# Performance work log

Hardware: AMD Instinct MI355X
Metric: run time of the kernel (lower is better)

The kernel has to match this reference:

```python
import jax, jax.numpy as jnp
import numpy as np

IGNORE_INDEX = -100


def setup_inputs() -> dict:
    key = jax.random.key(0)
    k1, k2, k3 = jax.random.split(key, 3)
    B, S, D, V = 4, 2048, 2048, 32000
    hidden_states = jax.random.normal(k1, (B, S, D), dtype=jnp.float32)
    lm_head_weight = jax.random.normal(k2, (V, D), dtype=jnp.float32) * (D ** -0.5)
    labels = jax.random.randint(k3, (B, S), 0, V, dtype=jnp.int64)
    return {"hidden_states": hidden_states, "lm_head_weight": lm_head_weight, "labels": labels}


def reference(hidden_states, lm_head_weight, labels):
    D = hidden_states.shape[-1]
    # causal LM shift: predict token t+1 from hidden state t
    h = hidden_states[..., :-1, :].astype(jnp.float32).reshape(-1, D)   # [N, D]
    t = labels[..., 1:].reshape(-1)                                     # [N]
    w = lm_head_weight.astype(jnp.float32)                              # [V, D]

    logits = jnp.einsum("nd,vd->nv", h, w)                              # [N, V]
    lse = jax.nn.logsumexp(logits, axis=-1)                             # [N]

    valid = t != IGNORE_INDEX
    safe_t = jnp.where(valid, t, 0)
    gold = jnp.take_along_axis(logits, safe_t[:, None], axis=-1)[:, 0]  # [N]

    nll = jnp.where(valid, lse - gold, 0.0)
    n_valid = jnp.maximum(jnp.sum(valid.astype(jnp.float32)), 1.0)
    return jnp.sum(nll) / n_valid
```

## Files before the change

kernel.cpp:

```cpp
#include <hip/hip_runtime.h>
#include <hip/hip_bf16.h>
#include <stdint.h>

#define IGNORE_INDEX (-100)

typedef __attribute__((ext_vector_type(8))) short bf16x8;
typedef __attribute__((ext_vector_type(4))) float f32x4;

static constexpr int Bv = 4, Sv = 2048, Dv = 2048, Vv = 32000;
static constexpr int Nv = Bv * (Sv - 1);
static constexpr int NP = 8192;
static constexpr int TILE = 128;
static constexpr int BK = 64;

typedef const __attribute__((address_space(1))) unsigned int* gptr_t;
typedef __attribute__((address_space(3))) unsigned int* lptr_t;

__device__ __forceinline__ unsigned short f2bf(float f) {
    unsigned int u = __float_as_uint(f);
    u += 0x7fffu + ((u >> 16) & 1u);
    return (unsigned short)(u >> 16);
}

__global__ void convert_w_kernel(const float* __restrict__ w,
                                 unsigned short* __restrict__ wbf) {
    int i = blockIdx.x * blockDim.x + threadIdx.x;
    const float4 v = ((const float4*)w)[i];
    ushort4 o;
    o.x = f2bf(v.x); o.y = f2bf(v.y); o.z = f2bf(v.z); o.w = f2bf(v.w);
    ((ushort4*)wbf)[i] = o;
}

__global__ void convert_h_kernel(const float* __restrict__ h,
                                 unsigned short* __restrict__ hbf) {
    int i = blockIdx.x * blockDim.x + threadIdx.x;
    int e0 = i * 4;
    int n = e0 >> 11;
    int d = e0 & 2047;
    ushort4 o;
    if (n < Nv) {
        int b = n / 2047;
        int s = n - b * 2047;
        const float4 v = *(const float4*)(h + ((size_t)b * Sv + s) * Dv + d);
        o.x = f2bf(v.x); o.y = f2bf(v.y); o.z = f2bf(v.z); o.w = f2bf(v.w);
    } else {
        o.x = 0; o.y = 0; o.z = 0; o.w = 0;
    }
    ((ushort4*)hbf)[i] = o;
}

__global__ void prep_meta_kernel(const int* __restrict__ labels,
                                 int* __restrict__ t,
                                 float* __restrict__ sumexp,
                                 float* __restrict__ gold) {
    int n = blockIdx.x * blockDim.x + threadIdx.x;
    if (n >= NP) return;
    sumexp[n] = 0.0f;
    gold[n] = 0.0f;
    int tv = IGNORE_INDEX;
    if (n < Nv) {
        int b = n / 2047;
        int s = n - b * 2047;
        tv = labels[b * Sv + s + 1];
    }
    t[n] = tv;
}

__global__ __launch_bounds__(256, 2)
void ce_gemm(const unsigned short* __restrict__ hbf,
             const unsigned short* __restrict__ wbf,
             const int* __restrict__ t,
             float* __restrict__ sumexp,
             float* __restrict__ gold) {
    __shared__ unsigned short lds_a[TILE * BK];
    __shared__ unsigned short lds_b[TILE * BK];
    __shared__ float lds_rowsum[TILE];
    __shared__ int lds_t[TILE];

    const int tid  = threadIdx.x;
    const int lane = tid & 63;
    const int wave = tid >> 6;
    const int r    = wave >> 1;
    const int c    = wave & 1;
    const int quad = lane >> 4;
    const int l15  = lane & 15;
    const int R0   = blockIdx.x * TILE;
    const int C0   = blockIdx.y * TILE;

    f32x4 acc[4][4];
    const f32x4 z = {0.f, 0.f, 0.f, 0.f};
#pragma unroll
    for (int mi = 0; mi < 4; ++mi)
#pragma unroll
        for (int ni = 0; ni < 4; ++ni)
            acc[mi][ni] = z;

    const int ld_r = tid >> 3;
    const int jg   = (tid & 7) ^ (ld_r & 7);
    const int ld_c = jg * 8;
    const unsigned short* ga = hbf + (size_t)(R0 + ld_r) * Dv + ld_c;
    const unsigned short* gb = wbf + (size_t)(C0 + ld_r) * Dv + ld_c;
    unsigned short* la = lds_a + tid * 8;
    unsigned short* lb = lds_b + tid * 8;

    for (int k0 = 0; k0 < Dv; k0 += BK) {
        __syncthreads();
#pragma unroll
        for (int i = 0; i < 4; ++i) {
            __builtin_amdgcn_global_load_lds(
                (gptr_t)(ga + (size_t)i * 32 * Dv + k0),
                (lptr_t)(la + i * 2048), 16, 0, 0);
            __builtin_amdgcn_global_load_lds(
                (gptr_t)(gb + (size_t)i * 32 * Dv + k0),
                (lptr_t)(lb + i * 2048), 16, 0, 0);
        }
        __syncthreads();
#pragma unroll
        for (int ks = 0; ks < BK; ks += 32) {
            bf16x8 af[4], bfr[4];
            const int cbase = quad + (ks >> 3);
#pragma unroll
            for (int mi = 0; mi < 4; ++mi) {
                const int arow = r * 64 + mi * 16 + l15;
                af[mi] = *(const bf16x8*)(lds_a + arow * BK + ((cbase ^ (arow & 7)) * 8));
            }
#pragma unroll
            for (int ni = 0; ni < 4; ++ni) {
                const int brow = c * 64 + ni * 16 + l15;
                bfr[ni] = *(const bf16x8*)(lds_b + brow * BK + ((cbase ^ (brow & 7)) * 8));
            }
#pragma unroll
            for (int mi = 0; mi < 4; ++mi)
#pragma unroll
                for (int ni = 0; ni < 4; ++ni)
                    acc[mi][ni] = __builtin_amdgcn_mfma_f32_16x16x32_bf16(
                        af[mi], bfr[ni], acc[mi][ni], 0, 0, 0);
        }
    }

    __syncthreads();
    if (tid < TILE) {
        lds_rowsum[tid] = 0.0f;
        lds_t[tid] = t[R0 + tid];
    }
    __syncthreads();

#pragma unroll
    for (int mi = 0; mi < 4; ++mi) {
#pragma unroll
        for (int reg = 0; reg < 4; ++reg) {
            const int lrow = r * 64 + mi * 16 + quad * 4 + reg;
            const int grow = R0 + lrow;
            const int lbl  = lds_t[lrow];
            float s = 0.0f;
#pragma unroll
            for (int ni = 0; ni < 4; ++ni) {
                const float v = acc[mi][ni][reg];
                s += __expf(v);
                const int gcol = C0 + c * 64 + ni * 16 + l15;
                if (lbl == gcol) gold[grow] = v;
            }
#pragma unroll
            for (int off = 1; off < 16; off <<= 1)
                s += __shfl_xor(s, off, 64);
            if (l15 == 0) atomicAdd(&lds_rowsum[lrow], s);
        }
    }
    __syncthreads();
    if (tid < TILE) {
        const int grow = R0 + tid;
        if (grow < Nv) atomicAdd(&sumexp[grow], lds_rowsum[tid]);
    }
}

__global__ void ce_finalize(const float* __restrict__ sumexp,
                            const float* __restrict__ gold,
                            const int* __restrict__ t,
                            float* __restrict__ out) {
    __shared__ float ssum[4];
    __shared__ float scnt[4];
    float s = 0.0f, cnt = 0.0f;
    for (int n = threadIdx.x; n < Nv; n += 256) {
        if (t[n] != IGNORE_INDEX) {
            s += logf(sumexp[n]) - gold[n];
            cnt += 1.0f;
        }
    }
#pragma unroll
    for (int off = 32; off > 0; off >>= 1) {
        s += __shfl_down(s, off, 64);
        cnt += __shfl_down(cnt, off, 64);
    }
    const int wid = threadIdx.x >> 6;
    if ((threadIdx.x & 63) == 0) { ssum[wid] = s; scnt[wid] = cnt; }
    __syncthreads();
    if (threadIdx.x == 0) {
        float S = 0.0f, C = 0.0f;
        for (int i = 0; i < 4; ++i) { S += ssum[i]; C += scnt[i]; }
        out[0] = S / fmaxf(C, 1.0f);
    }
}

extern "C" void kernel_launch(void* const* d_in, const int* in_sizes, int n_in,
                              void* d_out, int out_size, void* d_ws, size_t ws_size,
                              hipStream_t stream) {
    const float* h      = (const float*)d_in[0];
    const float* w      = (const float*)d_in[1];
    const int*   labels = (const int*)d_in[2];
    float* out = (float*)d_out;

    char* ws = (char*)d_ws;
    unsigned short* hbf = (unsigned short*)ws;
    unsigned short* wbf = (unsigned short*)(ws + (size_t)NP * Dv * 2);
    char* tail = ws + (size_t)NP * Dv * 2 + (size_t)Vv * Dv * 2;
    float* sumexp = (float*)tail;
    float* gold   = (float*)(tail + (size_t)NP * 4);
    int*   t      = (int*)(tail + (size_t)NP * 8);

    hipLaunchKernelGGL(convert_w_kernel, dim3((Vv * Dv / 4) / 256), dim3(256), 0, stream, w, wbf);
    hipLaunchKernelGGL(convert_h_kernel, dim3((NP * Dv / 4) / 256), dim3(256), 0, stream, h, hbf);
    hipLaunchKernelGGL(prep_meta_kernel, dim3(NP / 256), dim3(256), 0, stream, labels, t, sumexp, gold);
    hipLaunchKernelGGL(ce_gemm, dim3(NP / TILE, Vv / TILE), dim3(256), 0, stream,
                       hbf, wbf, t, sumexp, gold);
    hipLaunchKernelGGL(ce_finalize, dim3(1), dim3(256), 0, stream, sumexp, gold, t, out);
}
```

Measured before the change: 1.361 ms.

## Switch CE GEMM from bf16 to scaled FP8 MFMA 32x32x64

Converts hidden states and weights to FP8 (e4m3, with weights pre-scaled by 32) instead of bf16, and replaces the 16x16x32 bf16 MFMA with the scaled 32x32x64 f8f6f4 MFMA. A block scale of 2^-5 on B undoes the weight scaling. BK doubles to 128 bytes per row, and the epilogue is remapped to the 32x32 accumulator layout. The aim is to halve operand traffic and use the higher-throughput FP8 matrix path, at the cost of reduced precision in the logits, which may loosen accuracy on the loss.

```diff
diff --git a/kernel.cpp b/kernel.cpp
--- a/kernel.cpp
+++ b/kernel.cpp
@@ -4,49 +4,61 @@
 
 #define IGNORE_INDEX (-100)
 
-typedef __attribute__((ext_vector_type(8))) short bf16x8;
-typedef __attribute__((ext_vector_type(4))) float f32x4;
+typedef __attribute__((ext_vector_type(4)))  int   i32x4;
+typedef __attribute__((ext_vector_type(8)))  int   i32x8;
+typedef __attribute__((ext_vector_type(16))) float f32x16;
 
 static constexpr int Bv = 4, Sv = 2048, Dv = 2048, Vv = 32000;
 static constexpr int Nv = Bv * (Sv - 1);
 static constexpr int NP = 8192;
 static constexpr int TILE = 128;
-static constexpr int BK = 64;
+static constexpr int BK = 128;
+
+static constexpr int SCALE_A = 0x7F7F7F7F;
+static constexpr int SCALE_B = 0x7A7A7A7A;
 
 typedef const __attribute__((address_space(1))) unsigned int* gptr_t;
 typedef __attribute__((address_space(3))) unsigned int* lptr_t;
 
-__device__ __forceinline__ unsigned short f2bf(float f) {
-    unsigned int u = __float_as_uint(f);
-    u += 0x7fffu + ((u >> 16) & 1u);
-    return (unsigned short)(u >> 16);
+__device__ __forceinline__ int pack4_fp8(float a, float b, float c, float d) {
+    int v = __builtin_amdgcn_cvt_pk_fp8_f32(a, b, 0, false);
+    v = __builtin_amdgcn_cvt_pk_fp8_f32(c, d, v, true);
+    return v;
 }
 
 __global__ void convert_w_kernel(const float* __restrict__ w,
-                                 unsigned short* __restrict__ wbf) {
+                                 unsigned char* __restrict__ wf8) {
     int i = blockIdx.x * blockDim.x + threadIdx.x;
-    const float4 v = ((const float4*)w)[i];
-    ushort4 o;
-    o.x = f2bf(v.x); o.y = f2bf(v.y); o.z = f2bf(v.z); o.w = f2bf(v.w);
-    ((ushort4*)wbf)[i] = o;
+    const float4* src = (const float4*)w + i * 4;
+    i32x4 o;
+#pragma unroll
+    for (int j = 0; j < 4; ++j) {
+        const float4 v = src[j];
+        o[j] = pack4_fp8(v.x * 32.0f, v.y * 32.0f, v.z * 32.0f, v.w * 32.0f);
+    }
+    *(i32x4*)(wf8 + (size_t)i * 16) = o;
 }
 
 __global__ void convert_h_kernel(const float* __restrict__ h,
-                                 unsigned short* __restrict__ hbf) {
+                                 unsigned char* __restrict__ hf8) {
     int i = blockIdx.x * blockDim.x + threadIdx.x;
-    int e0 = i * 4;
+    int e0 = i * 16;
     int n = e0 >> 11;
     int d = e0 & 2047;
-    ushort4 o;
+    i32x4 o;
     if (n < Nv) {
         int b = n / 2047;
         int s = n - b * 2047;
-        const float4 v = *(const float4*)(h + ((size_t)b * Sv + s) * Dv + d);
-        o.x = f2bf(v.x); o.y = f2bf(v.y); o.z = f2bf(v.z); o.w = f2bf(v.w);
+        const float4* src = (const float4*)(h + ((size_t)b * Sv + s) * Dv + d);
+#pragma unroll
+        for (int j = 0; j < 4; ++j) {
+            const float4 v = src[j];
+            o[j] = pack4_fp8(v.x, v.y, v.z, v.w);
+        }
     } else {
-        o.x = 0; o.y = 0; o.z = 0; o.w = 0;
-    }
-    ((ushort4*)hbf)[i] = o;
+        o[0] = 0; o[1] = 0; o[2] = 0; o[3] = 0;
+    }
+    *(i32x4*)(hf8 + (size_t)i * 16) = o;
 }
 
 __global__ void prep_meta_kernel(const int* __restrict__ labels,
@@ -67,13 +79,13 @@
 }
 
 __global__ __launch_bounds__(256, 2)
-void ce_gemm(const unsigned short* __restrict__ hbf,
-             const unsigned short* __restrict__ wbf,
+void ce_gemm(const unsigned char* __restrict__ hf8,
+             const unsigned char* __restrict__ wf8,
              const int* __restrict__ t,
              float* __restrict__ sumexp,
              float* __restrict__ gold) {
-    __shared__ unsigned short lds_a[TILE * BK];
-    __shared__ unsigned short lds_b[TILE * BK];
+    __shared__ __align__(16) unsigned char lds_a[TILE * BK];
+    __shared__ __align__(16) unsigned char lds_b[TILE * BK];
     __shared__ float lds_rowsum[TILE];
     __shared__ int lds_t[TILE];
 
@@ -82,26 +94,26 @@
     const int wave = tid >> 6;
     const int r    = wave >> 1;
     const int c    = wave & 1;
-    const int quad = lane >> 4;
-    const int l15  = lane & 15;
+    const int l31  = lane & 31;
+    const int half = lane >> 5;
     const int R0   = blockIdx.x * TILE;
     const int C0   = blockIdx.y * TILE;
 
-    f32x4 acc[4][4];
-    const f32x4 z = {0.f, 0.f, 0.f, 0.f};
-#pragma unroll
-    for (int mi = 0; mi < 4; ++mi)
-#pragma unroll
-        for (int ni = 0; ni < 4; ++ni)
-            acc[mi][ni] = z;
+    f32x16 acc[2][2];
+#pragma unroll
+    for (int mi = 0; mi < 2; ++mi)
+#pragma unroll
+        for (int ni = 0; ni < 2; ++ni)
+#pragma unroll
+            for (int k = 0; k < 16; ++k)
+                acc[mi][ni][k] = 0.0f;
 
     const int ld_r = tid >> 3;
     const int jg   = (tid & 7) ^ (ld_r & 7);
-    const int ld_c = jg * 8;
-    const unsigned short* ga = hbf + (size_t)(R0 + ld_r) * Dv + ld_c;
-    const unsigned short* gb = wbf + (size_t)(C0 + ld_r) * Dv + ld_c;
-    unsigned short* la = lds_a + tid * 8;
-    unsigned short* lb = lds_b + tid * 8;
+    const unsigned char* ga = hf8 + (size_t)(R0 + ld_r) * Dv + jg * 16;
+    const unsigned char* gb = wf8 + (size_t)(C0 + ld_r) * Dv + jg * 16;
+    unsigned char* la = lds_a + tid * 16;
+    unsigned char* lb = lds_b + tid * 16;
 
     for (int k0 = 0; k0 < Dv; k0 += BK) {
         __syncthreads();
@@ -109,32 +121,41 @@
         for (int i = 0; i < 4; ++i) {
             __builtin_amdgcn_global_load_lds(
                 (gptr_t)(ga + (size_t)i * 32 * Dv + k0),
-                (lptr_t)(la + i * 2048), 16, 0, 0);
+                (lptr_t)(la + i * 4096), 16, 0, 0);
             __builtin_amdgcn_global_load_lds(
                 (gptr_t)(gb + (size_t)i * 32 * Dv + k0),
-                (lptr_t)(lb + i * 2048), 16, 0, 0);
+                (lptr_t)(lb + i * 4096), 16, 0, 0);
         }
         __syncthreads();
 #pragma unroll
-        for (int ks = 0; ks < BK; ks += 32) {
-            bf16x8 af[4], bfr[4];
-            const int cbase = quad + (ks >> 3);
-#pragma unroll
-            for (int mi = 0; mi < 4; ++mi) {
-                const int arow = r * 64 + mi * 16 + l15;
-                af[mi] = *(const bf16x8*)(lds_a + arow * BK + ((cbase ^ (arow & 7)) * 8));
+        for (int ks = 0; ks < BK; ks += 64) {
+            const int lc0 = (ks >> 4) + (half << 1);
+            union { i32x8 v8; i32x4 v4[2]; } af[2], bfr[2];
+#pragma unroll
+            for (int mi = 0; mi < 2; ++mi) {
+                const int ar = r * 64 + mi * 32 + l31;
+                const int sw = ar & 7;
+                const unsigned char* base = lds_a + ar * BK;
+                af[mi].v4[0] = *(const i32x4*)(base + ((lc0 ^ sw) * 16));
+                af[mi].v4[1] = *(const i32x4*)(base + (((lc0 + 1) ^ sw) * 16));
             }
 #pragma unroll
-            for (int ni = 0; ni < 4; ++ni) {
-                const int brow = c * 64 + ni * 16 + l15;
-                bfr[ni] = *(const bf16x8*)(lds_b + brow * BK + ((cbase ^ (brow & 7)) * 8));
+            for (int ni = 0; ni < 2; ++ni) {
+                const int br = c * 64 + ni * 32 + l31;
+                const int sw = br & 7;
+                const unsigned char* base = lds_b + br * BK;
+                bfr[ni].v4[0] = *(const i32x4*)(base + ((lc0 ^ sw) * 16));
+                bfr[ni].v4[1] = *(const i32x4*)(base + (((lc0 + 1) ^ sw) * 16));
             }
 #pragma unroll
-            for (int mi = 0; mi < 4; ++mi)
-#pragma unroll
-                for (int ni = 0; ni < 4; ++ni)
-                    acc[mi][ni] = __builtin_amdgcn_mfma_f32_16x16x32_bf16(
-                        af[mi], bfr[ni], acc[mi][ni], 0, 0, 0);
+            for (int mi = 0; mi < 2; ++mi)
+#pragma unroll
+                for (int ni = 0; ni < 2; ++ni)
+                    acc[mi][ni] = __builtin_amdgcn_mfma_scale_f32_32x32x64_f8f6f4(
+                        af[mi].v8, bfr[ni].v8, acc[mi][ni],
+                        0, 0,
+                        0, SCALE_A,
+                        0, SCALE_B);
         }
     }
 
@@ -146,24 +167,24 @@
     __syncthreads();
 
 #pragma unroll
-    for (int mi = 0; mi < 4; ++mi) {
-#pragma unroll
-        for (int reg = 0; reg < 4; ++reg) {
-            const int lrow = r * 64 + mi * 16 + quad * 4 + reg;
-            const int grow = R0 + lrow;
+    for (int mi = 0; mi < 2; ++mi) {
+#pragma unroll
+        for (int reg = 0; reg < 16; ++reg) {
+            const int row  = (reg & 3) + 8 * (reg >> 2) + 4 * half;
+            const int lrow = r * 64 + mi * 32 + row;
             const int lbl  = lds_t[lrow];
             float s = 0.0f;
 #pragma unroll
-            for (int ni = 0; ni < 4; ++ni) {
+            for (int ni = 0; ni < 2; ++ni) {
                 const float v = acc[mi][ni][reg];
                 s += __expf(v);
-                const int gcol = C0 + c * 64 + ni * 16 + l15;
-                if (lbl == gcol) gold[grow] = v;
+                const int gcol = C0 + c * 64 + ni * 32 + l31;
+                if (lbl == gcol) gold[R0 + lrow] = v;
             }
 #pragma unroll
-            for (int off = 1; off < 16; off <<= 1)
+            for (int off = 1; off < 32; off <<= 1)
                 s += __shfl_xor(s, off, 64);
-            if (l15 == 0) atomicAdd(&lds_rowsum[lrow], s);
+            if (l31 == 0) atomicAdd(&lds_rowsum[lrow], s);
         }
     }
     __syncthreads();
@@ -210,17 +231,17 @@
     float* out = (float*)d_out;
 
     char* ws = (char*)d_ws;
-    unsigned short* hbf = (unsigned short*)ws;
-    unsigned short* wbf = (unsigned short*)(ws + (size_t)NP * Dv * 2);
-    char* tail = ws + (size_t)NP * Dv * 2 + (size_t)Vv * Dv * 2;
+    unsigned char* hf8 = (unsigned char*)ws;
+    unsigned char* wf8 = (unsigned char*)(ws + (size_t)NP * Dv);
+    char* tail = ws + (size_t)NP * Dv + (size_t)Vv * Dv;
     float* sumexp = (float*)tail;
     float* gold   = (float*)(tail + (size_t)NP * 4);
     int*   t      = (int*)(tail + (size_t)NP * 8);
 
-    hipLaunchKernelGGL(convert_w_kernel, dim3((Vv * Dv / 4) / 256), dim3(256), 0, stream, w, wbf);
-    hipLaunchKernelGGL(convert_h_kernel, dim3((NP * Dv / 4) / 256), dim3(256), 0, stream, h, hbf);
+    hipLaunchKernelGGL(convert_w_kernel, dim3((Vv * Dv / 16) / 256), dim3(256), 0, stream, w, wf8);
+    hipLaunchKernelGGL(convert_h_kernel, dim3((NP * Dv / 16) / 256), dim3(256), 0, stream, h, hf8);
     hipLaunchKernelGGL(prep_meta_kernel, dim3(NP / 256), dim3(256), 0, stream, labels, t, sumexp, gold);
     hipLaunchKernelGGL(ce_gemm, dim3(NP / TILE, Vv / TILE), dim3(256), 0, stream,
-                       hbf, wbf, t, sumexp, gold);
+                       hf8, wf8, t, sumexp, gold);
     hipLaunchKernelGGL(ce_finalize, dim3(1), dim3(256), 0, stream, sumexp, gold, t, out);
 }
```

Result: slower. 4.980 ms (+266.0%).
